# Performance work log

Measured on AMD Instinct MI355X. Metric: run time of the kernel, lower is better.

## Reference

```python
import jax, jax.numpy as jnp
import numpy as np

EPS = 1e-15
B, N_PER, D, K, DEG = 64, 1024, 256, 64, 16  # graphs, nodes/graph, feat dim, pools/graph, avg degree


def setup_inputs() -> dict:
    key = jax.random.key(0)
    k1, k2, k3, k4 = jax.random.split(key, 4)
    N = B * N_PER
    E = B * N_PER * DEG
    x = jax.random.normal(k1, (N, D), jnp.float32)
    # edges confined within each graph (block-diagonal batched adjacency)
    rng = np.random.default_rng(0)
    offs = np.repeat(np.arange(B, dtype=np.int64) * N_PER, N_PER * DEG)
    src = rng.integers(0, N_PER, size=E) + offs
    dst = rng.integers(0, N_PER, size=E) + offs
    edge_index = jnp.asarray(np.stack([src, dst], axis=0), dtype=jnp.int32)
    edge_weight = jax.random.uniform(k2, (E,), jnp.float32)
    batch_ptr = jnp.arange(B + 1, dtype=jnp.int32) * N_PER
    W = jax.random.normal(k3, (D, K), jnp.float32) * 0.05  # pooling_net = Linear(D, K)
    b = jnp.zeros((K,), jnp.float32)
    gumbel_noise = jax.random.gumbel(k4, (N, K), jnp.float32)
    return {"x": x, "edge_weight": edge_weight, "W": W, "b": b,
            "gumbel_noise": gumbel_noise, "edge_index": edge_index, "batch_ptr": batch_ptr}


def _stochpool(x, edge_weight, W, b, gumbel_noise, edge_index, batch_ptr):
    N, Dd = x.shape
    nb = batch_ptr.shape[0] - 1          # num graphs
    n = N // nb                          # nodes per graph (equal-sized graphs)
    E = edge_index.shape[1]
    e_per = E // nb                      # edges per graph

    # pooling net + hard gumbel softmax (straight-through, tau=1)
    logits = x @ W + b                   # (N, K)
    y_soft = jax.nn.softmax(logits + gumbel_noise, axis=-1)
    y_hard = jax.nn.one_hot(jnp.argmax(y_soft, axis=-1), W.shape[1], dtype=y_soft.dtype)
    s = jax.lax.stop_gradient(y_hard - y_soft) + y_soft   # (N, K)

    u, v = edge_index[0], edge_index[1]
    graph_of_edge = u // n               # (E,) graph id per edge

    s_b = s.reshape(nb, n, -1)           # (B, n, K)
    x_b = x.reshape(nb, n, Dd)

    # pooled features: s^T x per graph
    out = jnp.einsum('bnk,bnd->bkd', s_b, x_b).reshape(nb * s_b.shape[2], Dd)

    # pooled adjacency: s^T A s per graph, via As = scatter-add over edges
    As = jnp.zeros_like(s).at[u].add(edge_weight[:, None] * s[v])   # (N, K) : (A s)
    out_adj = jnp.einsum('bnk,bnl->bkl', s_b, As.reshape(nb, n, -1))  # (B, K, K)

    # link loss: ||A - S S^T||_F per graph, via Frobenius expansion (no n x n dense)
    sq_A = jax.ops.segment_sum(edge_weight * edge_weight, graph_of_edge, num_segments=nb)
    cross = jax.ops.segment_sum(edge_weight * jnp.sum(s[u] * s[v], axis=-1),
                                graph_of_edge, num_segments=nb)
    StS = jnp.einsum('bnk,bnl->bkl', s_b, s_b)                # (B, K, K)
    sq_SSt = jnp.sum(StS * StS, axis=(1, 2))                  # ||S S^T||_F^2 = ||S^T S||_F^2
    link = jnp.sqrt(jnp.maximum(sq_A - 2.0 * cross + sq_SSt, 0.0))
    link = link / e_per                                       # normalize=True
    link_loss = jnp.mean(link)

    entropy_loss = jnp.mean(jnp.sum(-s * jnp.log(s + EPS), axis=-1))

    Kp = s_b.shape[2]
    batch = jnp.repeat(jnp.arange(nb, dtype=jnp.int32), Kp)
    batch_ptr_out = jnp.arange(0, (nb + 1) * Kp, Kp, dtype=jnp.int32)
    return out, out_adj, link_loss, entropy_loss, batch, batch_ptr_out


def reference(x, edge_weight, W, b, gumbel_noise, edge_index, batch_ptr):
    return _stochpool(x, edge_weight, W, b, gumbel_noise, edge_index, batch_ptr)
```

## Files before the change

### kernel.cpp

```cpp
#include <hip/hip_runtime.h>

#define NN 65536
#define DD 256
#define KK 64
#define NPG 1024

#define OUT_OFF   0
#define ADJ_OFF   1048576
#define LINK_OFF  1310720
#define ENT_OFF   1310721
#define BATCH_OFF 1310722
#define BPTR_OFF  1314818

#define WS_S1A    0
#define WS_C      524288
#define WS_SQP    540672
#define WS_CRP    544768
#define WS_ENTP   548864
#define WS_SORTP  552960
#define WS_GOFF   1077248
#define WS_ADJP   1093888
#define WS_NEED   (WS_ADJP + 1024 * 4096 * 4)

typedef __bf16 bf16x8 __attribute__((ext_vector_type(8)));
typedef unsigned short u16x8 __attribute__((ext_vector_type(8)));
typedef float f32x4 __attribute__((ext_vector_type(4)));

static __device__ __forceinline__ unsigned short f2bf(float f) {
  unsigned int u = __float_as_uint(f);
  return (unsigned short)((u + 0x7fffu + ((u >> 16) & 1u)) >> 16);
}

__global__ __launch_bounds__(256, 4) void pool_assign_kernel(
    const float* __restrict__ x, const float* __restrict__ Wm,
    const float* __restrict__ bvec, const float* __restrict__ gum,
    int2* __restrict__ s1a, float* __restrict__ entp)
{
  __shared__ unsigned short lds_wt[64 * 264];
  __shared__ float esum[4];
  const int t    = threadIdx.x;
  const int lane = t & 63;
  const int wv   = t >> 6;
  const int q    = lane >> 4;
  const int c    = lane & 15;
  const int nb0  = blockIdx.x << 6;

  #pragma unroll 8
  for (int i = 0; i < 64; ++i) {
    int idx = (i << 8) + t;
    lds_wt[(idx & 63) * 264 + (idx >> 6)] = f2bf(Wm[idx]);
  }

  const int arow = nb0 + (wv << 4) + c;
  const float* xrow = x + (size_t)arow * DD + (q << 3);
  u16x8 afr[8];
  #pragma unroll
  for (int kb = 0; kb < 8; ++kb) {
    float4 u0 = *(const float4*)(xrow + kb * 32);
    float4 u1 = *(const float4*)(xrow + kb * 32 + 4);
    u16x8 af;
    af[0] = f2bf(u0.x); af[1] = f2bf(u0.y); af[2] = f2bf(u0.z); af[3] = f2bf(u0.w);
    af[4] = f2bf(u1.x); af[5] = f2bf(u1.y); af[6] = f2bf(u1.z); af[7] = f2bf(u1.w);
    afr[kb] = af;
  }
  __syncthreads();

  f32x4 acc[4];
  #pragma unroll
  for (int n = 0; n < 4; ++n) acc[n] = (f32x4){0.f, 0.f, 0.f, 0.f};
  #pragma unroll
  for (int n = 0; n < 4; ++n) {
    #pragma unroll
    for (int kb = 0; kb < 8; ++kb) {
      u16x8 bu = *(const u16x8*)(&lds_wt[(n * 16 + c) * 264 + kb * 32 + (q << 3)]);
      acc[n] = __builtin_amdgcn_mfma_f32_16x16x32_bf16(
          __builtin_bit_cast(bf16x8, afr[kb]),
          __builtin_bit_cast(bf16x8, bu), acc[n], 0, 0, 0);
    }
  }

  float bb[4];
  #pragma unroll
  for (int n = 0; n < 4; ++n) bb[n] = bvec[n * 16 + c];
  const int nodeq = nb0 + (wv << 4) + (q << 2);
  float ent = 0.f;
  #pragma unroll
  for (int reg = 0; reg < 4; ++reg) {
    float zz[4];
    #pragma unroll
    for (int n = 0; n < 4; ++n)
      zz[n] = acc[n][reg] + bb[n] + gum[(size_t)(nodeq + reg) * KK + n * 16 + c];
    float m = zz[0]; int a = c;
    #pragma unroll
    for (int n = 1; n < 4; ++n)
      if (zz[n] > m) { m = zz[n]; a = n * 16 + c; }
    #pragma unroll
    for (int mask = 1; mask <= 8; mask <<= 1) {
      float mo = __shfl_xor(m, mask, 64);
      int   ao = __shfl_xor(a, mask, 64);
      if (mo > m || (mo == m && ao < a)) { m = mo; a = ao; }
    }
    float ls = 0.f;
    #pragma unroll
    for (int n = 0; n < 4; ++n) ls += expf(zz[n] - m);
    #pragma unroll
    for (int mask = 1; mask <= 8; mask <<= 1) ls += __shfl_xor(ls, mask, 64);
    if (c == 0) {
      int node = nodeq + reg;
      float p  = 1.0f / ls;
      float s1 = (1.0f - p) + p;
      s1a[node] = make_int2(a, __float_as_int(s1));
      ent += -s1 * logf(s1 + 1e-15f);
    }
  }
  #pragma unroll
  for (int off = 32; off; off >>= 1) ent += __shfl_down(ent, off, 64);
  if (lane == 0) esum[wv] = ent;
  __syncthreads();
  if (t == 0) entp[blockIdx.x] = esum[0] + esum[1] + esum[2] + esum[3];
}

__global__ __launch_bounds__(256) void sort_kernel(
    const int2* __restrict__ s1a, int2* __restrict__ sortedp,
    int* __restrict__ goff, float* __restrict__ c_out)
{
  __shared__ int hist[64];
  __shared__ int offs[65];
  __shared__ int cursor[64];
  const int t = threadIdx.x;
  const int g = blockIdx.x;
  const int n0 = g << 10;
  if (t < 64) hist[t] = 0;
  __syncthreads();
  int4 p01 = ((const int4*)(s1a + n0))[t * 2];
  int4 p23 = ((const int4*)(s1a + n0))[t * 2 + 1];
  atomicAdd(&hist[p01.x], 1);
  atomicAdd(&hist[p01.z], 1);
  atomicAdd(&hist[p23.x], 1);
  atomicAdd(&hist[p23.z], 1);
  __syncthreads();
  if (t == 0) {
    int s = 0;
    #pragma unroll
    for (int k = 0; k < 64; ++k) { offs[k] = s; s += hist[k]; }
    offs[64] = s;
  }
  __syncthreads();
  if (t < 64) cursor[t] = offs[t];
  if (t < 65) goff[g * 65 + t] = offs[t];
  __syncthreads();
  int p;
  p = atomicAdd(&cursor[p01.x], 1); sortedp[n0 + p] = make_int2(n0 + t * 4 + 0, p01.y);
  p = atomicAdd(&cursor[p01.z], 1); sortedp[n0 + p] = make_int2(n0 + t * 4 + 1, p01.w);
  p = atomicAdd(&cursor[p23.x], 1); sortedp[n0 + p] = make_int2(n0 + t * 4 + 2, p23.y);
  p = atomicAdd(&cursor[p23.z], 1); sortedp[n0 + p] = make_int2(n0 + t * 4 + 3, p23.w);
  __syncthreads();
  if (t < 64) {
    float cs = 0.f;
    int e = offs[t + 1];
    for (int o = offs[t]; o < e; ++o) {
      float v = __int_as_float(sortedp[n0 + o].y);
      cs += v * v;
    }
    c_out[(g << 6) + t] = cs;
  }
}

__global__ __launch_bounds__(256, 8) void fuse_ge_kernel(
    const float* __restrict__ x, const int2* __restrict__ sortedp,
    const int* __restrict__ goff, const int* __restrict__ src,
    const int* __restrict__ dst, const float* __restrict__ ew,
    const int2* __restrict__ s1a, float* __restrict__ out_feat,
    float* __restrict__ adjp, float* __restrict__ sqP, float* __restrict__ crP)
{
  __shared__ float adj[4096];
  __shared__ float redsq[4], redcr[4];
  const int t = threadIdx.x;
  if (blockIdx.x < 4096) {
    const int g = blockIdx.x >> 6;
    const int k = blockIdx.x & 63;
    const int o0 = goff[g * 65 + k];
    const int o1 = goff[g * 65 + k + 1];
    const int2* sp = sortedp + (g << 10);
    float sum = 0.f;
    int i = o0;
    for (; i + 4 <= o1; i += 4) {
      int2 e0 = sp[i], e1 = sp[i + 1], e2 = sp[i + 2], e3 = sp[i + 3];
      float x0 = x[(size_t)e0.x * DD + t];
      float x1 = x[(size_t)e1.x * DD + t];
      float x2 = x[(size_t)e2.x * DD + t];
      float x3 = x[(size_t)e3.x * DD + t];
      sum += __int_as_float(e0.y) * x0 + __int_as_float(e1.y) * x1
           + __int_as_float(e2.y) * x2 + __int_as_float(e3.y) * x3;
    }
    for (; i < o1; ++i) {
      int2 e = sp[i];
      sum += __int_as_float(e.y) * x[(size_t)e.x * DD + t];
    }
    out_feat[((size_t)(g * 64 + k)) * DD + t] = sum;
  } else {
    const int blk = blockIdx.x - 4096;
    const int g   = blk >> 4;
    #pragma unroll
    for (int i = 0; i < 16; ++i) adj[i * 256 + t] = 0.f;
    __syncthreads();
    const int e0 = blk << 10;
    float sq = 0.f, cr = 0.f;
    #pragma unroll
    for (int i = 0; i < 4; ++i) {
      int e = e0 + (i << 8) + t;
      int u = src[e], v = dst[e];
      float w = ew[e];
      int2 pu = s1a[u];
      int2 pv = s1a[v];
      float contrib = w * __int_as_float(pu.y) * __int_as_float(pv.y);
      atomicAdd(&adj[pu.x * 64 + pv.x], contrib);
      sq += w * w;
      if (pu.x == pv.x) cr += contrib;
    }
    #pragma unroll
    for (int off = 32; off; off >>= 1) {
      sq += __shfl_down(sq, off, 64);
      cr += __shfl_down(cr, off, 64);
    }
    if ((t & 63) == 0) { redsq[t >> 6] = sq; redcr[t >> 6] = cr; }
    __syncthreads();
    if (t == 0) {
      sqP[blk] = redsq[0] + redsq[1] + redsq[2] + redsq[3];
      crP[blk] = redcr[0] + redcr[1] + redcr[2] + redcr[3];
    }
    float* pp = adjp + (size_t)blk * 4096;
    #pragma unroll
    for (int i = 0; i < 16; ++i) pp[i * 256 + t] = adj[i * 256 + t];
    (void)g;
  }
}

__global__ __launch_bounds__(1024) void combine_fin_kernel(
    const float* __restrict__ adjp, const float* __restrict__ c,
    const float* __restrict__ sqP, const float* __restrict__ crP,
    const float* __restrict__ entp, float* __restrict__ out)
{
  __shared__ float ered[16];
  const int t = threadIdx.x;
  if (blockIdx.x < 256) {
    int idx = blockIdx.x * 1024 + t;
    int g = idx >> 12;
    int cell = idx & 4095;
    const float* p = adjp + ((size_t)(g * 16)) * 4096 + cell;
    float s = 0.f;
    #pragma unroll
    for (int j = 0; j < 16; ++j) s += p[j * 4096];
    out[ADJ_OFF + idx] = s;
    return;
  }
  float ent = entp[t];
  #pragma unroll
  for (int off = 32; off; off >>= 1) ent += __shfl_down(ent, off, 64);
  if ((t & 63) == 0) ered[t >> 6] = ent;
  float link = 0.f;
  if (t < 64) {
    const float* cg = c + t * 64;
    float ssq = 0.f;
    #pragma unroll
    for (int k = 0; k < 64; ++k) ssq += cg[k] * cg[k];
    float sq = 0.f, cr = 0.f;
    #pragma unroll
    for (int j = 0; j < 16; ++j) { sq += sqP[t * 16 + j]; cr += crP[t * 16 + j]; }
    float val = sq - 2.0f * cr + ssq;
    link = sqrtf(fmaxf(val, 0.f)) / 16384.0f;
    #pragma unroll
    for (int off = 32; off; off >>= 1) link += __shfl_down(link, off, 64);
  }
  __syncthreads();
  if (t == 0) {
    float es = 0.f;
    #pragma unroll
    for (int i = 0; i < 16; ++i) es += ered[i];
    out[LINK_OFF] = link / 64.0f;
    out[ENT_OFF]  = es / (float)NN;
  }
  for (int r = t; r < 4096; r += 1024) out[BATCH_OFF + r] = (float)(r >> 6);
  if (t < 65) out[BPTR_OFF + t] = (float)(t << 6);
}

__global__ __launch_bounds__(256) void edge_atomic_kernel(
    const int* __restrict__ src, const int* __restrict__ dst,
    const float* __restrict__ ew, const int2* __restrict__ s1a,
    float* __restrict__ out_adj, float* __restrict__ sqP, float* __restrict__ crP)
{
  __shared__ float adj[4096];
  __shared__ float redsq[4], redcr[4];
  const int t = threadIdx.x;
  const int blk = blockIdx.x;
  const int g = blk >> 4;
  #pragma unroll
  for (int i = 0; i < 16; ++i) adj[i * 256 + t] = 0.f;
  __syncthreads();
  const int e0 = blk << 10;
  float sq = 0.f, cr = 0.f;
  #pragma unroll
  for (int i = 0; i < 4; ++i) {
    int e = e0 + (i << 8) + t;
    int u = src[e], v = dst[e];
    float w = ew[e];
    int2 pu = s1a[u];
    int2 pv = s1a[v];
    float contrib = w * __int_as_float(pu.y) * __int_as_float(pv.y);
    atomicAdd(&adj[pu.x * 64 + pv.x], contrib);
    sq += w * w;
    if (pu.x == pv.x) cr += contrib;
  }
  #pragma unroll
  for (int off = 32; off; off >>= 1) {
    sq += __shfl_down(sq, off, 64);
    cr += __shfl_down(cr, off, 64);
  }
  if ((t & 63) == 0) { redsq[t >> 6] = sq; redcr[t >> 6] = cr; }
  __syncthreads();
  if (t == 0) {
    sqP[blk] = redsq[0] + redsq[1] + redsq[2] + redsq[3];
    crP[blk] = redcr[0] + redcr[1] + redcr[2] + redcr[3];
  }
  float* adjg = out_adj + (size_t)g * 4096;
  #pragma unroll
  for (int i = 0; i < 16; ++i) atomicAdd(&adjg[i * 256 + t], adj[i * 256 + t]);
}

__global__ __launch_bounds__(256, 8) void gather_kernel(
    const float* __restrict__ x, const int2* __restrict__ sortedp,
    const int* __restrict__ goff, float* __restrict__ out_feat)
{
  const int t = threadIdx.x;
  const int g = blockIdx.x >> 6;
  const int k = blockIdx.x & 63;
  const int o0 = goff[g * 65 + k];
  const int o1 = goff[g * 65 + k + 1];
  const int2* sp = sortedp + (g << 10);
  float sum = 0.f;
  for (int i = o0; i < o1; ++i) {
    int2 e = sp[i];
    sum += __int_as_float(e.y) * x[(size_t)e.x * DD + t];
  }
  out_feat[((size_t)(g * 64 + k)) * DD + t] = sum;
}

__global__ __launch_bounds__(1024) void finalize_only_kernel(
    const float* __restrict__ c, const float* __restrict__ sqP,
    const float* __restrict__ crP, const float* __restrict__ entp,
    float* __restrict__ out)
{
  __shared__ float ered[16];
  const int t = threadIdx.x;
  float ent = entp[t];
  #pragma unroll
  for (int off = 32; off; off >>= 1) ent += __shfl_down(ent, off, 64);
  if ((t & 63) == 0) ered[t >> 6] = ent;
  float link = 0.f;
  if (t < 64) {
    const float* cg = c + t * 64;
    float ssq = 0.f;
    #pragma unroll
    for (int k = 0; k < 64; ++k) ssq += cg[k] * cg[k];
    float sq = 0.f, cr = 0.f;
    #pragma unroll
    for (int j = 0; j < 16; ++j) { sq += sqP[t * 16 + j]; cr += crP[t * 16 + j]; }
    float val = sq - 2.0f * cr + ssq;
    link = sqrtf(fmaxf(val, 0.f)) / 16384.0f;
    #pragma unroll
    for (int off = 32; off; off >>= 1) link += __shfl_down(link, off, 64);
  }
  __syncthreads();
  if (t == 0) {
    float es = 0.f;
    #pragma unroll
    for (int i = 0; i < 16; ++i) es += ered[i];
    out[LINK_OFF] = link / 64.0f;
    out[ENT_OFF]  = es / (float)NN;
  }
  for (int r = t; r < 4096; r += 1024) out[BATCH_OFF + r] = (float)(r >> 6);
  if (t < 65) out[BPTR_OFF + t] = (float)(t << 6);
}

extern "C" void kernel_launch(void* const* d_in, const int* in_sizes, int n_in,
                              void* d_out, int out_size, void* d_ws, size_t ws_size,
                              hipStream_t stream) {
  const float* x    = (const float*)d_in[0];
  const float* ew   = (const float*)d_in[1];
  const float* Wm   = (const float*)d_in[2];
  const float* bvec = (const float*)d_in[3];
  const float* gum  = (const float*)d_in[4];
  const int*   eidx = (const int*)d_in[5];
  float* out = (float*)d_out;
  char*  ws  = (char*)d_ws;

  int2*  s1a     = (int2*)(ws + WS_S1A);
  float* c       = (float*)(ws + WS_C);
  float* sqP     = (float*)(ws + WS_SQP);
  float* crP     = (float*)(ws + WS_CRP);
  float* entp    = (float*)(ws + WS_ENTP);
  int2*  sortedp = (int2*)(ws + WS_SORTP);
  int*   goff    = (int*)(ws + WS_GOFF);
  float* adjp    = (float*)(ws + WS_ADJP);

  const int E = in_sizes[1];

  pool_assign_kernel<<<1024, 256, 0, stream>>>(x, Wm, bvec, gum, s1a, entp);
  sort_kernel<<<64, 256, 0, stream>>>(s1a, sortedp, goff, c);
  if (ws_size >= (size_t)WS_NEED) {
    fuse_ge_kernel<<<5120, 256, 0, stream>>>(x, sortedp, goff, eidx, eidx + E,
                                             ew, s1a, out + OUT_OFF, adjp, sqP, crP);
    combine_fin_kernel<<<257, 1024, 0, stream>>>(adjp, c, sqP, crP, entp, out);
  } else {
    hipMemsetAsync(out + ADJ_OFF, 0, (size_t)64 * 4096 * 4, stream);
    gather_kernel<<<4096, 256, 0, stream>>>(x, sortedp, goff, out + OUT_OFF);
    edge_atomic_kernel<<<1024, 256, 0, stream>>>(eidx, eidx + E, ew, s1a,
                                                 out + ADJ_OFF, sqP, crP);
    finalize_only_kernel<<<1, 1024, 0, stream>>>(c, sqP, crP, entp, out);
  }
}
```

Baseline: 60.52 us.

## Coarsen edge blocks, schedule them first, and compute per-bin sums in histogram pass

Each edge block now handles 4096 edges instead of 1024, so the workspace holds 4x fewer 64x64 partial adjacency tiles, and the combine step sums 4 partials per graph instead of 16. The edge-atomic blocks are placed at the front of the fused grid so the longer blocks start before the gather blocks. The sort kernel now accumulates per-bin squared assignment values with shared atomics during the histogram, replacing a serial 64-thread loop over the sorted output. In exchange there are fewer, longer edge blocks, which means less parallelism and more contention on the shared-memory atomics within each block.

```diff
diff --git a/kernel.cpp b/kernel.cpp
--- a/kernel.cpp
+++ b/kernel.cpp
@@ -15,12 +15,12 @@
 #define WS_S1A    0
 #define WS_C      524288
 #define WS_SQP    540672
-#define WS_CRP    544768
-#define WS_ENTP   548864
+#define WS_CRP    541696
+#define WS_ENTP   542720
 #define WS_SORTP  552960
 #define WS_GOFF   1077248
 #define WS_ADJP   1093888
-#define WS_NEED   (WS_ADJP + 1024 * 4096 * 4)
+#define WS_NEED   (WS_ADJP + 256 * 4096 * 4)
 
 typedef __bf16 bf16x8 __attribute__((ext_vector_type(8)));
 typedef unsigned short u16x8 __attribute__((ext_vector_type(8)));
@@ -127,10 +127,11 @@
   __shared__ int hist[64];
   __shared__ int offs[65];
   __shared__ int cursor[64];
+  __shared__ float cbin[64];
   const int t = threadIdx.x;
   const int g = blockIdx.x;
   const int n0 = g << 10;
-  if (t < 64) hist[t] = 0;
+  if (t < 64) { hist[t] = 0; cbin[t] = 0.f; }
   __syncthreads();
   int4 p01 = ((const int4*)(s1a + n0))[t * 2];
   int4 p23 = ((const int4*)(s1a + n0))[t * 2 + 1];
@@ -138,6 +139,12 @@
   atomicAdd(&hist[p01.z], 1);
   atomicAdd(&hist[p23.x], 1);
   atomicAdd(&hist[p23.z], 1);
+  float s0 = __int_as_float(p01.y), s1v = __int_as_float(p01.w);
+  float s2 = __int_as_float(p23.y), s3v = __int_as_float(p23.w);
+  atomicAdd(&cbin[p01.x], s0 * s0);
+  atomicAdd(&cbin[p01.z], s1v * s1v);
+  atomicAdd(&cbin[p23.x], s2 * s2);
+  atomicAdd(&cbin[p23.z], s3v * s3v);
   __syncthreads();
   if (t == 0) {
     int s = 0;
@@ -148,22 +155,13 @@
   __syncthreads();
   if (t < 64) cursor[t] = offs[t];
   if (t < 65) goff[g * 65 + t] = offs[t];
+  if (t < 64) c_out[(g << 6) + t] = cbin[t];
   __syncthreads();
   int p;
   p = atomicAdd(&cursor[p01.x], 1); sortedp[n0 + p] = make_int2(n0 + t * 4 + 0, p01.y);
   p = atomicAdd(&cursor[p01.z], 1); sortedp[n0 + p] = make_int2(n0 + t * 4 + 1, p01.w);
   p = atomicAdd(&cursor[p23.x], 1); sortedp[n0 + p] = make_int2(n0 + t * 4 + 2, p23.y);
   p = atomicAdd(&cursor[p23.z], 1); sortedp[n0 + p] = make_int2(n0 + t * 4 + 3, p23.w);
-  __syncthreads();
-  if (t < 64) {
-    float cs = 0.f;
-    int e = offs[t + 1];
-    for (int o = offs[t]; o < e; ++o) {
-      float v = __int_as_float(sortedp[n0 + o].y);
-      cs += v * v;
-    }
-    c_out[(g << 6) + t] = cs;
-  }
 }
 
 __global__ __launch_bounds__(256, 8) void fuse_ge_kernel(
@@ -176,9 +174,43 @@
   __shared__ float adj[4096];
   __shared__ float redsq[4], redcr[4];
   const int t = threadIdx.x;
-  if (blockIdx.x < 4096) {
-    const int g = blockIdx.x >> 6;
-    const int k = blockIdx.x & 63;
+  if (blockIdx.x < 256) {
+    const int blk = blockIdx.x;
+    #pragma unroll
+    for (int i = 0; i < 16; ++i) adj[i * 256 + t] = 0.f;
+    __syncthreads();
+    const int e0 = blk << 12;
+    float sq = 0.f, cr = 0.f;
+    #pragma unroll 4
+    for (int i = 0; i < 16; ++i) {
+      int e = e0 + (i << 8) + t;
+      int u = src[e], v = dst[e];
+      float w = ew[e];
+      int2 pu = s1a[u];
+      int2 pv = s1a[v];
+      float contrib = w * __int_as_float(pu.y) * __int_as_float(pv.y);
+      atomicAdd(&adj[pu.x * 64 + pv.x], contrib);
+      sq += w * w;
+      if (pu.x == pv.x) cr += contrib;
+    }
+    #pragma unroll
+    for (int off = 32; off; off >>= 1) {
+      sq += __shfl_down(sq, off, 64);
+      cr += __shfl_down(cr, off, 64);
+    }
+    if ((t & 63) == 0) { redsq[t >> 6] = sq; redcr[t >> 6] = cr; }
+    __syncthreads();
+    if (t == 0) {
+      sqP[blk] = redsq[0] + redsq[1] + redsq[2] + redsq[3];
+      crP[blk] = redcr[0] + redcr[1] + redcr[2] + redcr[3];
+    }
+    float* pp = adjp + (size_t)blk * 4096;
+    #pragma unroll
+    for (int i = 0; i < 16; ++i) pp[i * 256 + t] = adj[i * 256 + t];
+  } else {
+    const int bk = blockIdx.x - 256;
+    const int g = bk >> 6;
+    const int k = bk & 63;
     const int o0 = goff[g * 65 + k];
     const int o1 = goff[g * 65 + k + 1];
     const int2* sp = sortedp + (g << 10);
@@ -198,41 +230,6 @@
       sum += __int_as_float(e.y) * x[(size_t)e.x * DD + t];
     }
     out_feat[((size_t)(g * 64 + k)) * DD + t] = sum;
-  } else {
-    const int blk = blockIdx.x - 4096;
-    const int g   = blk >> 4;
-    #pragma unroll
-    for (int i = 0; i < 16; ++i) adj[i * 256 + t] = 0.f;
-    __syncthreads();
-    const int e0 = blk << 10;
-    float sq = 0.f, cr = 0.f;
-    #pragma unroll
-    for (int i = 0; i < 4; ++i) {
-      int e = e0 + (i << 8) + t;
-      int u = src[e], v = dst[e];
-      float w = ew[e];
-      int2 pu = s1a[u];
-      int2 pv = s1a[v];
-      float contrib = w * __int_as_float(pu.y) * __int_as_float(pv.y);
-      atomicAdd(&adj[pu.x * 64 + pv.x], contrib);
-      sq += w * w;
-      if (pu.x == pv.x) cr += contrib;
-    }
-    #pragma unroll
-    for (int off = 32; off; off >>= 1) {
-      sq += __shfl_down(sq, off, 64);
-      cr += __shfl_down(cr, off, 64);
-    }
-    if ((t & 63) == 0) { redsq[t >> 6] = sq; redcr[t >> 6] = cr; }
-    __syncthreads();
-    if (t == 0) {
-      sqP[blk] = redsq[0] + redsq[1] + redsq[2] + redsq[3];
-      crP[blk] = redcr[0] + redcr[1] + redcr[2] + redcr[3];
-    }
-    float* pp = adjp + (size_t)blk * 4096;
-    #pragma unroll
-    for (int i = 0; i < 16; ++i) pp[i * 256 + t] = adj[i * 256 + t];
-    (void)g;
   }
 }
 
@@ -247,11 +244,8 @@
     int idx = blockIdx.x * 1024 + t;
     int g = idx >> 12;
     int cell = idx & 4095;
-    const float* p = adjp + ((size_t)(g * 16)) * 4096 + cell;
-    float s = 0.f;
-    #pragma unroll
-    for (int j = 0; j < 16; ++j) s += p[j * 4096];
-    out[ADJ_OFF + idx] = s;
+    const float* p = adjp + ((size_t)(g * 4)) * 4096 + cell;
+    out[ADJ_OFF + idx] = p[0] + p[4096] + p[8192] + p[12288];
     return;
   }
   float ent = entp[t];
@@ -264,9 +258,8 @@
     float ssq = 0.f;
     #pragma unroll
     for (int k = 0; k < 64; ++k) ssq += cg[k] * cg[k];
-    float sq = 0.f, cr = 0.f;
-    #pragma unroll
-    for (int j = 0; j < 16; ++j) { sq += sqP[t * 16 + j]; cr += crP[t * 16 + j]; }
+    float sq = sqP[t * 4] + sqP[t * 4 + 1] + sqP[t * 4 + 2] + sqP[t * 4 + 3];
+    float cr = crP[t * 4] + crP[t * 4 + 1] + crP[t * 4 + 2] + crP[t * 4 + 3];
     float val = sq - 2.0f * cr + ssq;
     link = sqrtf(fmaxf(val, 0.f)) / 16384.0f;
     #pragma unroll
@@ -293,14 +286,14 @@
   __shared__ float redsq[4], redcr[4];
   const int t = threadIdx.x;
   const int blk = blockIdx.x;
-  const int g = blk >> 4;
+  const int g = blk >> 2;
   #pragma unroll
   for (int i = 0; i < 16; ++i) adj[i * 256 + t] = 0.f;
   __syncthreads();
-  const int e0 = blk << 10;
+  const int e0 = blk << 12;
   float sq = 0.f, cr = 0.f;
-  #pragma unroll
-  for (int i = 0; i < 4; ++i) {
+  #pragma unroll 4
+  for (int i = 0; i < 16; ++i) {
     int e = e0 + (i << 8) + t;
     int u = src[e], v = dst[e];
     float w = ew[e];
@@ -362,9 +355,8 @@
     float ssq = 0.f;
     #pragma unroll
     for (int k = 0; k < 64; ++k) ssq += cg[k] * cg[k];
-    float sq = 0.f, cr = 0.f;
-    #pragma unroll
-    for (int j = 0; j < 16; ++j) { sq += sqP[t * 16 + j]; cr += crP[t * 16 + j]; }
+    float sq = sqP[t * 4] + sqP[t * 4 + 1] + sqP[t * 4 + 2] + sqP[t * 4 + 3];
+    float cr = crP[t * 4] + crP[t * 4 + 1] + crP[t * 4 + 2] + crP[t * 4 + 3];
     float val = sq - 2.0f * cr + ssq;
     link = sqrtf(fmaxf(val, 0.f)) / 16384.0f;
     #pragma unroll
@@ -408,14 +400,14 @@
   pool_assign_kernel<<<1024, 256, 0, stream>>>(x, Wm, bvec, gum, s1a, entp);
   sort_kernel<<<64, 256, 0, stream>>>(s1a, sortedp, goff, c);
   if (ws_size >= (size_t)WS_NEED) {
-    fuse_ge_kernel<<<5120, 256, 0, stream>>>(x, sortedp, goff, eidx, eidx + E,
+    fuse_ge_kernel<<<4352, 256, 0, stream>>>(x, sortedp, goff, eidx, eidx + E,
                                              ew, s1a, out + OUT_OFF, adjp, sqP, crP);
     combine_fin_kernel<<<257, 1024, 0, stream>>>(adjp, c, sqP, crP, entp, out);
   } else {
     hipMemsetAsync(out + ADJ_OFF, 0, (size_t)64 * 4096 * 4, stream);
     gather_kernel<<<4096, 256, 0, stream>>>(x, sortedp, goff, out + OUT_OFF);
-    edge_atomic_kernel<<<1024, 256, 0, stream>>>(eidx, eidx + E, ew, s1a,
-                                                 out + ADJ_OFF, sqP, crP);
+    edge_atomic_kernel<<<256, 256, 0, stream>>>(eidx, eidx + E, ew, s1a,
+                                                out + ADJ_OFF, sqP, crP);
     finalize_only_kernel<<<1, 1024, 0, stream>>>(c, sqP, crP, entp, out);
   }
 }
```

New measurement: 49.19 us. 1.23x faster.
